# Kernel tuning notes

Measured on AMD Instinct MI355X. Metric: run time of the kernel, lower is better.

Reference implementation:

```python
import jax, jax.numpy as jnp
import numpy as np

N, E, D, B, C = 50000, 800000, 128, 20000, 40
EPS_BN = 1e-3    # keras BatchNormalization default epsilon
EPS_NRM = 1e-12  # keras ops.nn.normalize epsilon
FFN_DIMS = {"pre": (D, D), "c1p": (D, D), "c1u": (2 * D, D), "c2p": (D, D), "c2u": (2 * D, D), "post": (D, D)}


def setup_inputs() -> dict:
    key = jax.random.key(0)
    ks = jax.random.split(key, 8)
    inp = {
        "node_features": jax.random.normal(ks[0], (N, D), jnp.float32),
        "edges": jax.random.randint(ks[1], (2, E), 0, N, dtype=jnp.int32),
        "edge_w": jax.random.uniform(ks[2], (E,), jnp.float32),
        "input_node_idx": jax.random.randint(ks[3], (B,), 0, N, dtype=jnp.int32),
    }
    for i, (name, (din, dout)) in enumerate(FFN_DIMS.items()):
        kw = jax.random.fold_in(key, 100 + i)
        inp[name + "_g"] = jnp.ones((din,), jnp.float32)
        inp[name + "_be"] = jnp.zeros((din,), jnp.float32)
        inp[name + "_mu"] = jnp.zeros((din,), jnp.float32)
        inp[name + "_var"] = jnp.ones((din,), jnp.float32)
        inp[name + "_w"] = jax.random.normal(kw, (din, dout), jnp.float32) * (1.0 / float(np.sqrt(din)))
        inp[name + "_bi"] = jnp.zeros((dout,), jnp.float32)
    inp["logits_w"] = jax.random.normal(ks[4], (D, C), jnp.float32) * (1.0 / float(np.sqrt(D)))
    inp["logits_b"] = jnp.zeros((C,), jnp.float32)
    return inp


def ffn(x, g, be, mu, var, w, bi):
    # BatchNorm (inference running stats) -> Dropout (identity) -> Dense + exact gelu
    xn = (x - mu) * jax.lax.rsqrt(var + EPS_BN) * g + be
    return jax.nn.gelu(xn @ w + bi, approximate=False)


def l2norm(x):
    n = jnp.sqrt(jnp.sum(x * x, axis=-1, keepdims=True))
    return x / jnp.maximum(n, EPS_NRM)


def graph_conv(x, node_idx, nbr_idx, ew, prep, upd):
    # gather neighbours -> prepare FFN -> edge-weighted -> segment_sum (reduce='sum')
    msgs = ffn(x[nbr_idx], *prep) * ew[:, None]                         # [E, D]
    red = jax.ops.segment_sum(msgs, node_idx, num_segments=x.shape[0])  # [N, D]
    h = jnp.concatenate([x, red], axis=1)                               # [N, 2D] (combination='concat')
    return l2norm(ffn(h, *upd))                                         # normalize=True


def reference(node_features, edges, edge_w, input_node_idx,
              pre_g, pre_be, pre_mu, pre_var, pre_w, pre_bi,
              c1p_g, c1p_be, c1p_mu, c1p_var, c1p_w, c1p_bi,
              c1u_g, c1u_be, c1u_mu, c1u_var, c1u_w, c1u_bi,
              c2p_g, c2p_be, c2p_mu, c2p_var, c2p_w, c2p_bi,
              c2u_g, c2u_be, c2u_mu, c2u_var, c2u_w, c2u_bi,
              post_g, post_be, post_mu, post_var, post_w, post_bi,
              logits_w, logits_b):
    ew = edge_w / jnp.sum(edge_w)                       # edge_W normalized at init
    node_idx, nbr_idx = edges[0], edges[1]
    x = ffn(node_features, pre_g, pre_be, pre_mu, pre_var, pre_w, pre_bi)
    x = graph_conv(x, node_idx, nbr_idx, ew,
                   (c1p_g, c1p_be, c1p_mu, c1p_var, c1p_w, c1p_bi),
                   (c1u_g, c1u_be, c1u_mu, c1u_var, c1u_w, c1u_bi)) + x
    x = graph_conv(x, node_idx, nbr_idx, ew,
                   (c2p_g, c2p_be, c2p_mu, c2p_var, c2p_w, c2p_bi),
                   (c2u_g, c2u_be, c2u_mu, c2u_var, c2u_w, c2u_bi)) + x
    x = ffn(x, post_g, post_be, post_mu, post_var, post_w, post_bi)
    return x[input_node_idx] @ logits_w + logits_b      # [B, C]
```

## Files before the change

kernel.cpp:

```cpp
#include <hip/hip_runtime.h>
#include <hip/hip_fp16.h>
#include <math.h>

static constexpr int D = 128;
static constexpr int CAP = 64;
static constexpr float EPS_BN = 1e-3f;

typedef short short8 __attribute__((ext_vector_type(8)));
typedef short short4v __attribute__((ext_vector_type(4)));
typedef float float4v __attribute__((ext_vector_type(4)));

__device__ __forceinline__ float gelu_exact(float x) {
    return 0.5f * x * (1.0f + erff(x * 0.70710678118654752f));
}

__device__ __forceinline__ void f32_to_hilo(float f, short& h, short& l) {
    unsigned u = __float_as_uint(f);
    h = (short)(u >> 16);
    float hf = __uint_as_float(u & 0xFFFF0000u);
    unsigned lu = __float_as_uint(f - hf);
    l = (short)(lu >> 16);
}

__device__ __forceinline__ short f32_to_bf16_rne(float f) {
    unsigned u = __float_as_uint(f);
    u += 0x7FFFu + ((u >> 16) & 1u);
    return (short)(u >> 16);
}

__device__ __forceinline__ void cvt_hilo8(const float4& x, const float4& y, short8& h8, short8& l8) {
    short h, l;
    f32_to_hilo(x.x, h, l); h8[0] = h; l8[0] = l;
    f32_to_hilo(x.y, h, l); h8[1] = h; l8[1] = l;
    f32_to_hilo(x.z, h, l); h8[2] = h; l8[2] = l;
    f32_to_hilo(x.w, h, l); h8[3] = h; l8[3] = l;
    f32_to_hilo(y.x, h, l); h8[4] = h; l8[4] = l;
    f32_to_hilo(y.y, h, l); h8[5] = h; l8[5] = l;
    f32_to_hilo(y.z, h, l); h8[6] = h; l8[6] = l;
    f32_to_hilo(y.w, h, l); h8[7] = h; l8[7] = l;
}

__device__ __forceinline__ short8 cvt_rne8(const float4& x, const float4& y) {
    short8 r;
    r[0] = f32_to_bf16_rne(x.x); r[1] = f32_to_bf16_rne(x.y);
    r[2] = f32_to_bf16_rne(x.z); r[3] = f32_to_bf16_rne(x.w);
    r[4] = f32_to_bf16_rne(y.x); r[5] = f32_to_bf16_rne(y.y);
    r[6] = f32_to_bf16_rne(y.z); r[7] = f32_to_bf16_rne(y.w);
    return r;
}

struct FoldArgs {
    const float* g[6]; const float* be[6]; const float* mu[6];
    const float* var[6]; const float* w[6]; const float* bi[6];
    short* wh[6]; short* wl[6]; float* bp[6]; int K[6];
};

__global__ void k_fold(FoldArgs fa) {
    __shared__ float sm[4];
    const int tid = threadIdx.x;
    const int lane = tid & 63, wvi = tid >> 6;
    const int f = blockIdx.x >> 7;
    const int c = blockIdx.x & 127;
    const int K = fa.K[f];
    const float* g = fa.g[f]; const float* be = fa.be[f];
    const float* mu = fa.mu[f]; const float* var = fa.var[f];
    const float* w = fa.w[f]; const float* bi = fa.bi[f];
    short* wh = fa.wh[f]; short* wl = fa.wl[f]; float* bp = fa.bp[f];
    float part = 0.f;
    for (int k = tid; k < K; k += blockDim.x) {
        float a = g[k] / sqrtf(var[k] + EPS_BN);
        float wv = w[k * D + c];
        float prod = a * wv;
        short hh, ll;
        f32_to_hilo(prod, hh, ll);
        wh[c * K + k] = hh;
        wl[c * K + k] = ll;
        part += (be[k] - mu[k] * a) * wv;
    }
    for (int off = 32; off > 0; off >>= 1) part += __shfl_down(part, off, 64);
    if (lane == 0) sm[wvi] = part;
    __syncthreads();
    if (tid == 0) bp[c] = bi[c] + sm[0] + sm[1] + sm[2] + sm[3];
}

__global__ void __launch_bounds__(512) k_fillpre(
    const int* __restrict__ edges, const float* __restrict__ ew,
    int* __restrict__ cnt, float* __restrict__ sums, unsigned* __restrict__ cw,
    int E, int N,
    const float* __restrict__ A0, const short* __restrict__ Wh,
    const short* __restrict__ Wl, const float* __restrict__ bp,
    float* __restrict__ outf)
{
    constexpr int K = 128;
    constexpr int WSZ = 128 * K;
    __shared__ short Wlds[2 * WSZ];
    __shared__ float sm[8];

    const int tid = threadIdx.x;
    const int lane = tid & 63;
    const int wvi = tid >> 6;

    const int grp = blockIdx.x >> 8;
    const int role = grp & 1;
    const int rid = ((grp >> 1) << 8) | (blockIdx.x & 255);

    if (role == 0) {
        const int g = rid & 7;
        const int bid = rid >> 3;
        const int gstride = 64 * 512;
        const int N8 = (N + 7) >> 3;
        const int lo = g * N8;
        const int hi = min(lo + N8, N);
        float s = 0.f;
        for (int e = bid * 512 + tid; e < E; e += gstride) {
            int dst = edges[e];
            if (dst >= lo && dst < hi) {
                int src = edges[E + e];
                float w = ew[e];
                s += w;
                unsigned short wb = __half_as_ushort(__float2half(w));
                int idx = atomicAdd(&cnt[dst], 1);
                if (idx < CAP)
                    cw[(size_t)dst * CAP + idx] = ((unsigned)src << 16) | (unsigned)wb;
            }
        }
        for (int off = 32; off > 0; off >>= 1) s += __shfl_down(s, off, 64);
        if (lane == 0) sm[wvi] = s;
        __syncthreads();
        if (tid == 0) {
            float t = 0.f;
            #pragma unroll
            for (int i = 0; i < 8; i++) t += sm[i];
            if (t != 0.f) atomicAdd(sums, t);
        }
        return;
    }

    const int fbid = rid;
    constexpr int NBLK = 512;

    #pragma unroll
    for (int it = 0; it < (2 * WSZ) / (512 * 8); ++it) {
        int s = it * 4096 + tid * 8;
        int buf = s / WSZ;
        int rem = s - buf * WSZ;
        int c = rem / K;
        int kk = (rem & (K - 1)) ^ ((c & 7) << 3);
        const short* src = (buf ? Wl : Wh) + c * K + kk;
        *(short8*)&Wlds[s] = *(const short8*)src;
    }
    __syncthreads();

    const int wv = tid >> 6;
    const int ssub = wv >> 2;
    const int wc = wv & 3;
    const int m = lane & 15;
    const int quad = lane >> 4;
    const int nstrips = (N + 15) >> 4;
    const int stride = NBLK * 2;

    for (int strip = fbid * 2 + ssub; strip < nstrips; strip += stride) {
        int r = strip * 16 + m;
        if (r >= N) r = N - 1;
        const float* pA0 = A0 + (size_t)r * D;

        float4 a[2][4];
        {
            const float4* s4 = (const float4*)pA0 + quad * 2;
            a[0][0] = s4[0]; a[0][1] = s4[1]; a[0][2] = s4[8]; a[0][3] = s4[9];
        }
        {
            const float4* s4 = (const float4*)(pA0 + 64) + quad * 2;
            a[1][0] = s4[0]; a[1][1] = s4[1]; a[1][2] = s4[8]; a[1][3] = s4[9];
        }

        float4v acc[2];
        acc[0] = (float4v){0.f, 0.f, 0.f, 0.f};
        acc[1] = (float4v){0.f, 0.f, 0.f, 0.f};

        #pragma unroll
        for (int cc = 0; cc < 2; ++cc) {
            #pragma unroll
            for (int ks = 0; ks < 2; ++ks) {
                const int kk = cc * 64 + ks * 32 + quad * 8;
                short8 ah, al;
                cvt_hilo8(a[cc][ks * 2], a[cc][ks * 2 + 1], ah, al);
                #pragma unroll
                for (int tj = 0; tj < 2; ++tj) {
                    const int c = wc * 32 + tj * 16 + m;
                    const int idx = c * K + (kk ^ ((c & 7) << 3));
                    short8 bh = *(const short8*)&Wlds[idx];
                    short8 bl = *(const short8*)&Wlds[WSZ + idx];
                    acc[tj] = __builtin_amdgcn_mfma_f32_16x16x32_bf16(al, bh, acc[tj], 0, 0, 0);
                    acc[tj] = __builtin_amdgcn_mfma_f32_16x16x32_bf16(ah, bl, acc[tj], 0, 0, 0);
                    acc[tj] = __builtin_amdgcn_mfma_f32_16x16x32_bf16(ah, bh, acc[tj], 0, 0, 0);
                }
            }
        }

        #pragma unroll
        for (int tj = 0; tj < 2; ++tj) {
            float bv = bp[wc * 32 + tj * 16 + m];
            #pragma unroll
            for (int r4 = 0; r4 < 4; ++r4)
                acc[tj][r4] = gelu_exact(acc[tj][r4] + bv);
        }
        #pragma unroll
        for (int r4 = 0; r4 < 4; ++r4) {
            int row = strip * 16 + quad * 4 + r4;
            if (row < N) {
                #pragma unroll
                for (int tj = 0; tj < 2; ++tj) {
                    int col = wc * 32 + tj * 16 + m;
                    outf[(size_t)row * D + col] = acc[tj][r4];
                }
            }
        }
    }
}

__device__ __forceinline__ void accum8(float* acc, const float4& raw, float w) {
    const __half2* hp = (const __half2*)&raw;
    #pragma unroll
    for (int t = 0; t < 4; t++) {
        float2 f = __half22float2(hp[t]);
        acc[t * 2]     += w * f.x;
        acc[t * 2 + 1] += w * f.y;
    }
}

__global__ void k_reduce(const int* __restrict__ cnt, const unsigned* __restrict__ cw,
                         const float* __restrict__ sums, const __half* __restrict__ y,
                         float* __restrict__ red, int N) {
    int n = blockIdx.x * (blockDim.x >> 6) + (threadIdx.x >> 6);
    if (n >= N) return;
    float inv = 1.0f / sums[0];
    int lane = threadIdx.x & 63;
    int sub = lane >> 4;
    int q = lane & 15;
    int count = min(cnt[n], CAP);
    int start = n * CAP;
    int end = start + count;
    float acc[8] = {0.f, 0.f, 0.f, 0.f, 0.f, 0.f, 0.f, 0.f};
    int i = start + sub;
    for (; i + 12 < end; i += 16) {
        unsigned c0 = cw[i];
        unsigned c1 = cw[i + 4];
        unsigned c2 = cw[i + 8];
        unsigned c3 = cw[i + 12];
        float4 r0 = *((const float4*)(y + (size_t)(c0 >> 16) * D) + q);
        float4 r1 = *((const float4*)(y + (size_t)(c1 >> 16) * D) + q);
        float4 r2 = *((const float4*)(y + (size_t)(c2 >> 16) * D) + q);
        float4 r3 = *((const float4*)(y + (size_t)(c3 >> 16) * D) + q);
        float w0 = __half2float(__ushort_as_half((unsigned short)(c0 & 0xFFFFu))) * inv;
        float w1 = __half2float(__ushort_as_half((unsigned short)(c1 & 0xFFFFu))) * inv;
        float w2 = __half2float(__ushort_as_half((unsigned short)(c2 & 0xFFFFu))) * inv;
        float w3 = __half2float(__ushort_as_half((unsigned short)(c3 & 0xFFFFu))) * inv;
        accum8(acc, r0, w0);
        accum8(acc, r1, w1);
        accum8(acc, r2, w2);
        accum8(acc, r3, w3);
    }
    for (; i < end; i += 4) {
        unsigned c = cw[i];
        float4 r = *((const float4*)(y + (size_t)(c >> 16) * D) + q);
        float w = __half2float(__ushort_as_half((unsigned short)(c & 0xFFFFu))) * inv;
        accum8(acc, r, w);
    }
    #pragma unroll
    for (int t = 0; t < 8; t++) {
        acc[t] += __shfl_xor(acc[t], 16, 64);
        acc[t] += __shfl_xor(acc[t], 32, 64);
    }
    if (sub == 0) {
        float4 o0 = {acc[0], acc[1], acc[2], acc[3]};
        float4 o1 = {acc[4], acc[5], acc[6], acc[7]};
        *((float4*)(red + (size_t)n * D + q * 8)) = o0;
        *((float4*)(red + (size_t)n * D + q * 8 + 4)) = o1;
    }
}

template<int K, bool SPLIT3, bool L2RES, bool OUT16, bool GATHER>
__global__ void __launch_bounds__(512) k_ffn(
    const float* __restrict__ A0, const float* __restrict__ A1,
    const short* __restrict__ Wh, const short* __restrict__ Wl,
    const float* __restrict__ bp, const float* __restrict__ resid,
    float* __restrict__ outf, __half* __restrict__ outh, int N,
    const int* __restrict__ gidx)
{
    constexpr int NB = SPLIT3 ? 2 : 1;
    constexpr int WSZ = 128 * K;
    constexpr int NC = K / 64;
    __shared__ short Wlds[NB * WSZ];
    __shared__ float rsum[2][16][4];

    const int tid = threadIdx.x;

    constexpr int ITER = (NB * WSZ) / (512 * 8);
    #pragma unroll
    for (int it = 0; it < ITER; ++it) {
        int s = it * 4096 + tid * 8;
        int buf = s / WSZ;
        int rem = s - buf * WSZ;
        int c = rem / K;
        int kk = (rem & (K - 1)) ^ ((c & 7) << 3);
        const short* src = (buf ? Wl : Wh) + c * K + kk;
        *(short8*)&Wlds[s] = *(const short8*)src;
    }
    __syncthreads();

    const int lane = tid & 63;
    const int wv = tid >> 6;
    const int ssub = wv >> 2;
    const int wc = wv & 3;
    const int m = lane & 15;
    const int quad = lane >> 4;
    const int nstrips = (N + 15) >> 4;
    const int stride = gridDim.x * 2;
    const int base = blockIdx.x * 2 + ssub;

    auto body = [&](int strip, bool active) {
        int rr = active ? strip * 16 + m : m;
        if (rr >= N) rr = N - 1;
        const int r = GATHER ? gidx[rr] : rr;
        const float* pA0 = A0 + (size_t)r * D;
        const float* pA1 = (K == 256) ? (A1 + (size_t)r * D) : pA0;

        float4 a[2][4];
        {
            const float4* s4 = (const float4*)pA0 + quad * 2;
            a[0][0] = s4[0]; a[0][1] = s4[1]; a[0][2] = s4[8]; a[0][3] = s4[9];
        }
        {
            const float4* s4 = (const float4*)(pA0 + 64) + quad * 2;
            a[1][0] = s4[0]; a[1][1] = s4[1]; a[1][2] = s4[8]; a[1][3] = s4[9];
        }

        float4v acc[2];
        acc[0] = (float4v){0.f, 0.f, 0.f, 0.f};
        acc[1] = (float4v){0.f, 0.f, 0.f, 0.f};

        #pragma unroll
        for (int cc = 0; cc < NC; ++cc) {
            #pragma unroll
            for (int ks = 0; ks < 2; ++ks) {
                const int kk = cc * 64 + ks * 32 + quad * 8;
                short8 ah, al;
                if (SPLIT3) cvt_hilo8(a[cc & 1][ks * 2], a[cc & 1][ks * 2 + 1], ah, al);
                else        ah = cvt_rne8(a[cc & 1][ks * 2], a[cc & 1][ks * 2 + 1]);
                #pragma unroll
                for (int tj = 0; tj < 2; ++tj) {
                    const int c = wc * 32 + tj * 16 + m;
                    const int idx = c * K + (kk ^ ((c & 7) << 3));
                    short8 bh = *(const short8*)&Wlds[idx];
                    if (SPLIT3) {
                        short8 bl = *(const short8*)&Wlds[WSZ + idx];
                        acc[tj] = __builtin_amdgcn_mfma_f32_16x16x32_bf16(al, bh, acc[tj], 0, 0, 0);
                        acc[tj] = __builtin_amdgcn_mfma_f32_16x16x32_bf16(ah, bl, acc[tj], 0, 0, 0);
                    }
                    acc[tj] = __builtin_amdgcn_mfma_f32_16x16x32_bf16(ah, bh, acc[tj], 0, 0, 0);
                }
            }
            if (cc + 2 < NC) {
                const int n2 = cc + 2;
                const float* src = (K == 256 && n2 >= 2) ? pA1 : pA0;
                const int kb = (K == 256) ? ((n2 & 1) * 64) : (n2 * 64);
                const float4* s4 = (const float4*)(src + kb) + quad * 2;
                a[cc & 1][0] = s4[0]; a[cc & 1][1] = s4[1];
                a[cc & 1][2] = s4[8]; a[cc & 1][3] = s4[9];
            }
        }

        #pragma unroll
        for (int tj = 0; tj < 2; ++tj) {
            float bv = bp[wc * 32 + tj * 16 + m];
            #pragma unroll
            for (int r4 = 0; r4 < 4; ++r4)
                acc[tj][r4] = gelu_exact(acc[tj][r4] + bv);
        }

        if (L2RES) {
            float ss[4];
            #pragma unroll
            for (int r4 = 0; r4 < 4; ++r4) {
                float v = acc[0][r4] * acc[0][r4] + acc[1][r4] * acc[1][r4];
                v += __shfl_xor(v, 1, 64);
                v += __shfl_xor(v, 2, 64);
                v += __shfl_xor(v, 4, 64);
                v += __shfl_xor(v, 8, 64);
                ss[r4] = v;
            }
            if (m == 0) {
                #pragma unroll
                for (int r4 = 0; r4 < 4; ++r4) rsum[ssub][quad * 4 + r4][wc] = ss[r4];
            }
            __syncthreads();
            #pragma unroll
            for (int r4 = 0; r4 < 4; ++r4) {
                const int rib = quad * 4 + r4;
                float tot = rsum[ssub][rib][0] + rsum[ssub][rib][1]
                          + rsum[ssub][rib][2] + rsum[ssub][rib][3];
                float inv = 1.0f / fmaxf(sqrtf(tot), 1e-12f);
                int row = strip * 16 + rib;
                if (active && row < N) {
                    #pragma unroll
                    for (int tj = 0; tj < 2; ++tj) {
                        int col = wc * 32 + tj * 16 + m;
                        outf[(size_t)row * D + col] = acc[tj][r4] * inv + resid[(size_t)row * D + col];
                    }
                }
            }
            __syncthreads();
        } else {
            #pragma unroll
            for (int r4 = 0; r4 < 4; ++r4) {
                int row = strip * 16 + quad * 4 + r4;
                if (active && row < N) {
                    #pragma unroll
                    for (int tj = 0; tj < 2; ++tj) {
                        int col = wc * 32 + tj * 16 + m;
                        if (OUT16) outh[(size_t)row * D + col] = __float2half(acc[tj][r4]);
                        else       outf[(size_t)row * D + col] = acc[tj][r4];
                    }
                }
            }
        }
    };

    if (L2RES) {
        int rem = nstrips - blockIdx.x * 2;
        int nit = rem > 0 ? (rem + stride - 1) / stride : 0;
        for (int it = 0; it < nit; ++it) {
            int strip = base + it * stride;
            body(strip, strip < nstrips);
        }
    } else {
        for (int strip = base; strip < nstrips; strip += stride)
            body(strip, true);
    }
}

__global__ void k_logits(const float* __restrict__ x,
                         const float* __restrict__ LW, const float* __restrict__ lb,
                         float* __restrict__ out, int B) {
    int wid = blockIdx.x * 4 + (threadIdx.x >> 6);
    int lane = threadIdx.x & 63;
    if (wid >= B) return;
    if (lane >= 40) return;
    float acc = lb[lane];
    const float4* xr = (const float4*)(x + (size_t)wid * D);
    #pragma unroll 4
    for (int k4 = 0; k4 < 32; k4++) {
        float4 xv = xr[k4];
        acc += xv.x * LW[(4 * k4 + 0) * 40 + lane];
        acc += xv.y * LW[(4 * k4 + 1) * 40 + lane];
        acc += xv.z * LW[(4 * k4 + 2) * 40 + lane];
        acc += xv.w * LW[(4 * k4 + 3) * 40 + lane];
    }
    out[(size_t)wid * 40 + lane] = acc;
}

extern "C" void kernel_launch(void* const* d_in, const int* in_sizes, int n_in,
                              void* d_out, int out_size, void* d_ws, size_t ws_size,
                              hipStream_t stream) {
    const float* node_features = (const float*)d_in[0];
    const int*   edges         = (const int*)d_in[1];
    const float* edge_w        = (const float*)d_in[2];
    const int*   input_idx     = (const int*)d_in[3];
    const int N = in_sizes[0] / D;
    const int E = in_sizes[2];
    const int B = in_sizes[3];

    const float* P[6][6];
    for (int f = 0; f < 6; f++)
        for (int q = 0; q < 6; q++)
            P[f][q] = (const float*)d_in[4 + f * 6 + q];
    const float* logits_w = (const float*)d_in[40];
    const float* logits_b = (const float*)d_in[41];

    float* ws = (float*)d_ws;
    size_t nd = (size_t)N * D;
    float* xA  = ws;
    float* y   = ws + nd;
    float* red = ws + 2 * nd;
    float* p   = ws + 3 * nd;
    __half* yh = (__half*)p; p += nd / 2;
    const int Ks[6] = {128, 128, 256, 128, 256, 128};
    short* Wh[6]; short* Wl[6]; float* Bp[6];
    {
        short* sp = (short*)p;
        for (int f = 0; f < 6; f++) {
            Wh[f] = sp; sp += (size_t)Ks[f] * D;
            Wl[f] = sp; sp += (size_t)Ks[f] * D;
        }
        p = (float*)sp;
    }
    for (int f = 0; f < 6; f++) { Bp[f] = p; p += D; }
    int* cnt    = (int*)p; p += N;
    float* sums = p; p += 2;
    unsigned* cw = (unsigned*)p; p += (size_t)N * CAP;

    FoldArgs fa;
    for (int f = 0; f < 6; f++) {
        fa.g[f] = P[f][0]; fa.be[f] = P[f][1]; fa.mu[f] = P[f][2];
        fa.var[f] = P[f][3]; fa.w[f] = P[f][4]; fa.bi[f] = P[f][5];
        fa.wh[f] = Wh[f]; fa.wl[f] = Wl[f]; fa.bp[f] = Bp[f]; fa.K[f] = Ks[f];
    }

    hipMemsetAsync(cnt, 0, ((size_t)N + 2) * sizeof(int), stream);
    k_fold<<<768, 256, 0, stream>>>(fa);
    k_fillpre<<<1024, 512, 0, stream>>>(edges, edge_w, cnt, sums, cw, E, N,
                                        node_features, Wh[0], Wl[0], Bp[0], xA);

    const int rb = (N + 3) / 4;
    const int g1 = 256;
    const int g2 = 512;
    const int g3 = 1024;

    k_ffn<128, false, false, true,  false><<<g3, 512, 0, stream>>>(xA, nullptr, Wh[1], Wl[1], Bp[1], nullptr, nullptr, yh, N, nullptr);
    k_reduce<<<rb, 256, 0, stream>>>(cnt, cw, sums, yh, red, N);
    k_ffn<256, true,  true,  false, false><<<g1, 512, 0, stream>>>(xA, red, Wh[2], Wl[2], Bp[2], xA, y, nullptr, N, nullptr);
    k_ffn<128, false, false, true,  false><<<g3, 512, 0, stream>>>(y, nullptr, Wh[3], Wl[3], Bp[3], nullptr, nullptr, yh, N, nullptr);
    k_reduce<<<rb, 256, 0, stream>>>(cnt, cw, sums, yh, red, N);
    k_ffn<256, true,  true,  false, false><<<g1, 512, 0, stream>>>(y, red, Wh[4], Wl[4], Bp[4], y, xA, nullptr, N, nullptr);
    k_ffn<128, true,  false, false, true ><<<g2, 512, 0, stream>>>(xA, nullptr, Wh[5], Wl[5], Bp[5], nullptr, red, nullptr, B, input_idx);
    k_logits<<<(B + 3) / 4, 256, 0, stream>>>(red, logits_w, logits_b, (float*)d_out, B);
}
```

Baseline: 443.6 us.

## Fuse conv1 prepare FFN into fillpre kernel and widen K=256 update blocks

The pre-FFN output of each strip is staged as bf16 in LDS and immediately multiplied by the conv1 prepare weights (single bf16 MFMA, weights read from global), writing yh directly. This removes one kernel launch and a full re-read of xA. The K=256 update FFN kernels are also templated on block size and launched with 1024 threads so four strips share one LDS weight load. Risks: the prepare GEMM now uses only the high bf16 part of the weights and a bf16-rounded input, which lowers precision, and it reads weights uncached from global memory with extra barriers.

```diff
diff --git a/kernel.cpp b/kernel.cpp
--- a/kernel.cpp
+++ b/kernel.cpp
@@ -89,11 +89,14 @@
     int E, int N,
     const float* __restrict__ A0, const short* __restrict__ Wh,
     const short* __restrict__ Wl, const float* __restrict__ bp,
-    float* __restrict__ outf)
+    float* __restrict__ outf,
+    const short* __restrict__ Wh1, const float* __restrict__ bp1,
+    __half* __restrict__ yh)
 {
     constexpr int K = 128;
     constexpr int WSZ = 128 * K;
     __shared__ short Wlds[2 * WSZ];
+    __shared__ short xbuf[2][16][136];
     __shared__ float sm[8];
 
     const int tid = threadIdx.x;
@@ -137,7 +140,6 @@
     }
 
     const int fbid = rid;
-    constexpr int NBLK = 512;
 
     #pragma unroll
     for (int it = 0; it < (2 * WSZ) / (512 * 8); ++it) {
@@ -157,65 +159,111 @@
     const int m = lane & 15;
     const int quad = lane >> 4;
     const int nstrips = (N + 15) >> 4;
-    const int stride = NBLK * 2;
-
-    for (int strip = fbid * 2 + ssub; strip < nstrips; strip += stride) {
-        int r = strip * 16 + m;
-        if (r >= N) r = N - 1;
-        const float* pA0 = A0 + (size_t)r * D;
-
-        float4 a[2][4];
-        {
-            const float4* s4 = (const float4*)pA0 + quad * 2;
-            a[0][0] = s4[0]; a[0][1] = s4[1]; a[0][2] = s4[8]; a[0][3] = s4[9];
-        }
-        {
-            const float4* s4 = (const float4*)(pA0 + 64) + quad * 2;
-            a[1][0] = s4[0]; a[1][1] = s4[1]; a[1][2] = s4[8]; a[1][3] = s4[9];
-        }
-
+
+    int remw = nstrips - fbid * 2;
+    int nit = remw > 0 ? (remw + 1023) / 1024 : 0;
+
+    for (int it = 0; it < nit; ++it) {
+        const int strip = fbid * 2 + ssub + it * 1024;
+        const bool active = strip < nstrips;
         float4v acc[2];
         acc[0] = (float4v){0.f, 0.f, 0.f, 0.f};
         acc[1] = (float4v){0.f, 0.f, 0.f, 0.f};
 
-        #pragma unroll
-        for (int cc = 0; cc < 2; ++cc) {
-            #pragma unroll
-            for (int ks = 0; ks < 2; ++ks) {
-                const int kk = cc * 64 + ks * 32 + quad * 8;
-                short8 ah, al;
-                cvt_hilo8(a[cc][ks * 2], a[cc][ks * 2 + 1], ah, al);
-                #pragma unroll
-                for (int tj = 0; tj < 2; ++tj) {
-                    const int c = wc * 32 + tj * 16 + m;
-                    const int idx = c * K + (kk ^ ((c & 7) << 3));
-                    short8 bh = *(const short8*)&Wlds[idx];
-                    short8 bl = *(const short8*)&Wlds[WSZ + idx];
-                    acc[tj] = __builtin_amdgcn_mfma_f32_16x16x32_bf16(al, bh, acc[tj], 0, 0, 0);
-                    acc[tj] = __builtin_amdgcn_mfma_f32_16x16x32_bf16(ah, bl, acc[tj], 0, 0, 0);
-                    acc[tj] = __builtin_amdgcn_mfma_f32_16x16x32_bf16(ah, bh, acc[tj], 0, 0, 0);
-                }
-            }
-        }
-
-        #pragma unroll
-        for (int tj = 0; tj < 2; ++tj) {
-            float bv = bp[wc * 32 + tj * 16 + m];
-            #pragma unroll
-            for (int r4 = 0; r4 < 4; ++r4)
-                acc[tj][r4] = gelu_exact(acc[tj][r4] + bv);
-        }
-        #pragma unroll
-        for (int r4 = 0; r4 < 4; ++r4) {
-            int row = strip * 16 + quad * 4 + r4;
-            if (row < N) {
+        if (active) {
+            int r = strip * 16 + m;
+            if (r >= N) r = N - 1;
+            const float* pA0 = A0 + (size_t)r * D;
+
+            float4 a[2][4];
+            {
+                const float4* s4 = (const float4*)pA0 + quad * 2;
+                a[0][0] = s4[0]; a[0][1] = s4[1]; a[0][2] = s4[8]; a[0][3] = s4[9];
+            }
+            {
+                const float4* s4 = (const float4*)(pA0 + 64) + quad * 2;
+                a[1][0] = s4[0]; a[1][1] = s4[1]; a[1][2] = s4[8]; a[1][3] = s4[9];
+            }
+
+            #pragma unroll
+            for (int cc = 0; cc < 2; ++cc) {
+                #pragma unroll
+                for (int ks = 0; ks < 2; ++ks) {
+                    const int kk = cc * 64 + ks * 32 + quad * 8;
+                    short8 ah, al;
+                    cvt_hilo8(a[cc][ks * 2], a[cc][ks * 2 + 1], ah, al);
+                    #pragma unroll
+                    for (int tj = 0; tj < 2; ++tj) {
+                        const int c = wc * 32 + tj * 16 + m;
+                        const int idx = c * K + (kk ^ ((c & 7) << 3));
+                        short8 bh = *(const short8*)&Wlds[idx];
+                        short8 bl = *(const short8*)&Wlds[WSZ + idx];
+                        acc[tj] = __builtin_amdgcn_mfma_f32_16x16x32_bf16(al, bh, acc[tj], 0, 0, 0);
+                        acc[tj] = __builtin_amdgcn_mfma_f32_16x16x32_bf16(ah, bl, acc[tj], 0, 0, 0);
+                        acc[tj] = __builtin_amdgcn_mfma_f32_16x16x32_bf16(ah, bh, acc[tj], 0, 0, 0);
+                    }
+                }
+            }
+
+            #pragma unroll
+            for (int tj = 0; tj < 2; ++tj) {
+                float bv = bp[wc * 32 + tj * 16 + m];
+                #pragma unroll
+                for (int r4 = 0; r4 < 4; ++r4)
+                    acc[tj][r4] = gelu_exact(acc[tj][r4] + bv);
+            }
+            #pragma unroll
+            for (int r4 = 0; r4 < 4; ++r4) {
+                int rib = quad * 4 + r4;
+                int row = strip * 16 + rib;
                 #pragma unroll
                 for (int tj = 0; tj < 2; ++tj) {
                     int col = wc * 32 + tj * 16 + m;
-                    outf[(size_t)row * D + col] = acc[tj][r4];
-                }
-            }
-        }
+                    if (row < N) outf[(size_t)row * D + col] = acc[tj][r4];
+                    xbuf[ssub][rib][col] = f32_to_bf16_rne(acc[tj][r4]);
+                }
+            }
+        }
+        __syncthreads();
+
+        if (active) {
+            float4v acc2[2];
+            acc2[0] = (float4v){0.f, 0.f, 0.f, 0.f};
+            acc2[1] = (float4v){0.f, 0.f, 0.f, 0.f};
+            #pragma unroll
+            for (int cc = 0; cc < 2; ++cc) {
+                #pragma unroll
+                for (int ks = 0; ks < 2; ++ks) {
+                    const int kk = cc * 64 + ks * 32 + quad * 8;
+                    short8 ah = *(const short8*)&xbuf[ssub][m][kk];
+                    #pragma unroll
+                    for (int tj = 0; tj < 2; ++tj) {
+                        const int c = wc * 32 + tj * 16 + m;
+                        short8 bh = *(const short8*)(Wh1 + (size_t)c * 128 + kk);
+                        acc2[tj] = __builtin_amdgcn_mfma_f32_16x16x32_bf16(ah, bh, acc2[tj], 0, 0, 0);
+                    }
+                }
+            }
+            #pragma unroll
+            for (int tj = 0; tj < 2; ++tj) {
+                float bv = bp1[wc * 32 + tj * 16 + m];
+                #pragma unroll
+                for (int r4 = 0; r4 < 4; ++r4)
+                    acc2[tj][r4] = gelu_exact(acc2[tj][r4] + bv);
+            }
+            #pragma unroll
+            for (int r4 = 0; r4 < 4; ++r4) {
+                int row = strip * 16 + quad * 4 + r4;
+                if (row < N) {
+                    #pragma unroll
+                    for (int tj = 0; tj < 2; ++tj) {
+                        int col = wc * 32 + tj * 16 + m;
+                        yh[(size_t)row * D + col] = __float2half(acc2[tj][r4]);
+                    }
+                }
+            }
+        }
+        __syncthreads();
     }
 }
 
@@ -280,8 +328,8 @@
     }
 }
 
-template<int K, bool SPLIT3, bool L2RES, bool OUT16, bool GATHER>
-__global__ void __launch_bounds__(512) k_ffn(
+template<int K, int BLOCK, bool SPLIT3, bool L2RES, bool OUT16, bool GATHER>
+__global__ void __launch_bounds__(BLOCK, BLOCK / 256) k_ffn(
     const float* __restrict__ A0, const float* __restrict__ A1,
     const short* __restrict__ Wh, const short* __restrict__ Wl,
     const float* __restrict__ bp, const float* __restrict__ resid,
@@ -291,15 +339,16 @@
     constexpr int NB = SPLIT3 ? 2 : 1;
     constexpr int WSZ = 128 * K;
     constexpr int NC = K / 64;
+    constexpr int SS = BLOCK / 256;
     __shared__ short Wlds[NB * WSZ];
-    __shared__ float rsum[2][16][4];
+    __shared__ float rsum[SS][16][4];
 
     const int tid = threadIdx.x;
 
-    constexpr int ITER = (NB * WSZ) / (512 * 8);
+    constexpr int ITER = (NB * WSZ) / (BLOCK * 8);
     #pragma unroll
     for (int it = 0; it < ITER; ++it) {
-        int s = it * 4096 + tid * 8;
+        int s = it * (BLOCK * 8) + tid * 8;
         int buf = s / WSZ;
         int rem = s - buf * WSZ;
         int c = rem / K;
@@ -316,8 +365,8 @@
     const int m = lane & 15;
     const int quad = lane >> 4;
     const int nstrips = (N + 15) >> 4;
-    const int stride = gridDim.x * 2;
-    const int base = blockIdx.x * 2 + ssub;
+    const int stride = gridDim.x * SS;
+    const int base = blockIdx.x * SS + ssub;
 
     auto body = [&](int strip, bool active) {
         int rr = active ? strip * 16 + m : m;
@@ -428,7 +477,7 @@
     };
 
     if (L2RES) {
-        int rem = nstrips - blockIdx.x * 2;
+        int rem = nstrips - blockIdx.x * SS;
         int nit = rem > 0 ? (rem + stride - 1) / stride : 0;
         for (int it = 0; it < nit; ++it) {
             int strip = base + it * stride;
@@ -510,19 +559,19 @@
     hipMemsetAsync(cnt, 0, ((size_t)N + 2) * sizeof(int), stream);
     k_fold<<<768, 256, 0, stream>>>(fa);
     k_fillpre<<<1024, 512, 0, stream>>>(edges, edge_w, cnt, sums, cw, E, N,
-                                        node_features, Wh[0], Wl[0], Bp[0], xA);
+                                        node_features, Wh[0], Wl[0], Bp[0], xA,
+                                        Wh[1], Bp[1], yh);
 
     const int rb = (N + 3) / 4;
     const int g1 = 256;
     const int g2 = 512;
     const int g3 = 1024;
 
-    k_ffn<128, false, false, true,  false><<<g3, 512, 0, stream>>>(xA, nullptr, Wh[1], Wl[1], Bp[1], nullptr, nullptr, yh, N, nullptr);
     k_reduce<<<rb, 256, 0, stream>>>(cnt, cw, sums, yh, red, N);
-    k_ffn<256, true,  true,  false, false><<<g1, 512, 0, stream>>>(xA, red, Wh[2], Wl[2], Bp[2], xA, y, nullptr, N, nullptr);
-    k_ffn<128, false, false, true,  false><<<g3, 512, 0, stream>>>(y, nullptr, Wh[3], Wl[3], Bp[3], nullptr, nullptr, yh, N, nullptr);
+    k_ffn<256, 1024, true,  true,  false, false><<<g1, 1024, 0, stream>>>(xA, red, Wh[2], Wl[2], Bp[2], xA, y, nullptr, N, nullptr);
+    k_ffn<128, 512,  false, false, true,  false><<<g3, 512, 0, stream>>>(y, nullptr, Wh[3], Wl[3], Bp[3], nullptr, nullptr, yh, N, nullptr);
     k_reduce<<<rb, 256, 0, stream>>>(cnt, cw, sums, yh, red, N);
-    k_ffn<256, true,  true,  false, false><<<g1, 512, 0, stream>>>(y, red, Wh[4], Wl[4], Bp[4], y, xA, nullptr, N, nullptr);
-    k_ffn<128, true,  false, false, true ><<<g2, 512, 0, stream>>>(xA, nullptr, Wh[5], Wl[5], Bp[5], nullptr, red, nullptr, B, input_idx);
+    k_ffn<256, 1024, true,  true,  false, false><<<g1, 1024, 0, stream>>>(y, red, Wh[4], Wl[4], Bp[4], y, xA, nullptr, N, nullptr);
+    k_ffn<128, 512,  true,  false, false, true ><<<g2, 512, 0, stream>>>(xA, nullptr, Wh[5], Wl[5], Bp[5], nullptr, red, nullptr, B, input_idx);
     k_logits<<<(B + 3) / 4, 256, 0, stream>>>(red, logits_w, logits_b, (float*)d_out, B);
 }
```

Measured after the change: 435.1 us. About the same (-1.9%).
